# Kernel optimization log

Hardware: AMD Instinct MI355X
Metric: run time of the kernel (lower is better)

## Reference

```python
import jax, jax.numpy as jnp
import numpy as np
import math

H = 16
D_MODEL = 1024
D_K = 64
BS = 8
SEQ = 1024


def setup_inputs() -> dict:
    key = jax.random.key(0)
    ks = jax.random.split(key, 13)
    s = 1.0 / math.sqrt(D_MODEL)
    inp = {
        "q": jax.random.normal(ks[0], (BS, SEQ, D_MODEL), dtype=jnp.float32),
        "k": jax.random.normal(ks[1], (BS, SEQ, D_MODEL), dtype=jnp.float32),
        "v": jax.random.normal(ks[2], (BS, SEQ, D_MODEL), dtype=jnp.float32),
        "mask": jax.random.randint(ks[3], (BS, SEQ, SEQ), 0, 2, dtype=jnp.int32),
        "Wq": jax.random.normal(ks[4], (D_MODEL, D_MODEL), dtype=jnp.float32) * s,
        "bq": jax.random.normal(ks[5], (D_MODEL,), dtype=jnp.float32) * s,
        "Wk": jax.random.normal(ks[6], (D_MODEL, D_MODEL), dtype=jnp.float32) * s,
        "bk": jax.random.normal(ks[7], (D_MODEL,), dtype=jnp.float32) * s,
        "Wv": jax.random.normal(ks[8], (D_MODEL, D_MODEL), dtype=jnp.float32) * s,
        "bv": jax.random.normal(ks[9], (D_MODEL,), dtype=jnp.float32) * s,
        "Wo": jax.random.normal(ks[10], (D_MODEL, D_MODEL), dtype=jnp.float32) * s,
        "bo": jax.random.normal(ks[11], (D_MODEL,), dtype=jnp.float32) * s,
    }
    return inp


def reference(q, k, v, mask, Wq, bq, Wk, bk, Wv, bv, Wo, bo):
    bs, seq, _ = q.shape
    # projections, split heads: [b, h, s, dk]
    def proj(x, W, b):
        y = x @ W + b
        return y.reshape(bs, seq, H, D_K).transpose(0, 2, 1, 3)
    qh = proj(q, Wq, bq)
    kh = proj(k, Wk, bk)
    vh = proj(v, Wv, bv)
    # scaled dot-product attention (dropout is identity in eval mode)
    scores = jnp.einsum("bhqd,bhkd->bhqk", qh, kh) / math.sqrt(D_K)
    scores = jnp.where(mask[:, None, :, :] == 0, jnp.float32(-1e9), scores)
    attn = jax.nn.softmax(scores, axis=-1)
    ctx = jnp.einsum("bhqk,bhkd->bhqd", attn, vh)
    concat = ctx.transpose(0, 2, 1, 3).reshape(bs, seq, D_MODEL)
    return concat @ Wo + bo
```

## Files before the change

### kernel.cpp

```cpp
#include <hip/hip_runtime.h>
#include <hip/hip_bf16.h>

#define HN 16
#define DM 1024
#define DK 64
#define BSZ 8
#define SEQL 1024

typedef __attribute__((ext_vector_type(8))) short bf16x8;
typedef __attribute__((ext_vector_type(4))) short short4v;
typedef __attribute__((ext_vector_type(4))) float f32x4;

__device__ __forceinline__ short f2bf(float f) {
    union { float f; unsigned u; } x; x.f = f;
    unsigned u = x.u + 0x7FFFu + ((x.u >> 16) & 1u);
    return (short)(u >> 16);
}

__device__ __forceinline__ void async16(const void* g, void* ldsbase) {
    __builtin_amdgcn_global_load_lds(
        (const __attribute__((address_space(1))) unsigned int*)g,
        (__attribute__((address_space(3))) unsigned int*)ldsbase, 16, 0, 0);
}

__device__ __forceinline__ short4v pack4bf(float v0, float v1, float v2, float v3) {
    unsigned pk0, pk1;
    asm("v_cvt_pk_bf16_f32 %0, %1, %2" : "=v"(pk0) : "v"(v0), "v"(v1));
    asm("v_cvt_pk_bf16_f32 %0, %1, %2" : "=v"(pk1) : "v"(v2), "v"(v3));
    union { unsigned u[2]; short4v s4; } u_;
    u_.u[0] = pk0; u_.u[1] = pk1;
    return u_.s4;
}

__device__ __forceinline__ bf16x8 pack8bf(f32x4 lo, f32x4 hi) {
    union { short4v h[2]; bf16x8 v; } u_;
    u_.h[0] = pack4bf(lo.x, lo.y, lo.z, lo.w);
    u_.h[1] = pack4bf(hi.x, hi.y, hi.z, hi.w);
    return u_.v;
}

__global__ __launch_bounds__(256) void transpose_cast4(const float* __restrict__ W0,
                                                       const float* __restrict__ W1,
                                                       const float* __restrict__ W2,
                                                       const float* __restrict__ W3,
                                                       short* __restrict__ T0,
                                                       short* __restrict__ T1,
                                                       short* __restrict__ T2,
                                                       short* __restrict__ T3) {
    __shared__ float tile[32][33];
    const int zi = blockIdx.z;
    const float* W = zi == 0 ? W0 : zi == 1 ? W1 : zi == 2 ? W2 : W3;
    short* Wt = zi == 0 ? T0 : zi == 1 ? T1 : zi == 2 ? T2 : T3;
    const int t = threadIdx.x;
    const int k0 = blockIdx.x * 32, n0 = blockIdx.y * 32;
    const int c = t & 31, r = t >> 5;
    #pragma unroll
    for (int p = 0; p < 4; ++p)
        tile[r + 8 * p][c] = W[(size_t)(k0 + r + 8 * p) * DM + n0 + c];
    __syncthreads();
    #pragma unroll
    for (int p = 0; p < 4; ++p)
        Wt[(size_t)(n0 + r + 8 * p) * DM + k0 + c] = f2bf(tile[c][r + 8 * p]);
}

__global__ __launch_bounds__(256) void pack_mask(const int* __restrict__ mask,
                                                 unsigned short* __restrict__ bt) {
    size_t gi = (size_t)blockIdx.x * 256 + threadIdx.x;
    size_t word = gi >> 6;
    int l = threadIdx.x & 63;
    int jperm = ((l >> 2) & 3) * 16 + ((l >> 4) & 3) * 4 + (l & 3);
    size_t row = word >> 4;
    int jblk = (int)(word & 15);
    unsigned long long b = __ballot(mask[row * SEQL + jblk * 64 + jperm] != 0);
    if (l < 4)
        bt[row * 64 + l * 16 + jblk] = (unsigned short)(b >> (l * 16));
}

__global__ __launch_bounds__(256) void gemm_qkv(
    const float* __restrict__ Aq, const float* __restrict__ Ak,
    const float* __restrict__ Av,
    const short* __restrict__ Wqt, const short* __restrict__ Wkt,
    const short* __restrict__ Wvt,
    const float* __restrict__ bqp, const float* __restrict__ bkp,
    const float* __restrict__ bvp,
    short* __restrict__ Cq, short* __restrict__ Ck, short* __restrict__ Cv,
    int zlog) {
    __shared__ __attribute__((aligned(16))) float Af[2][128][32];
    __shared__ __attribute__((aligned(16))) short Bs[2][128][32];
    const int t = threadIdx.x;
    const int lane = t & 63, wv = t >> 6;
    const int wm = (wv >> 1) * 64, wn = (wv & 1) * 64;
    const int quad = lane >> 4, l15 = lane & 15;
    const int tileM = blockIdx.x * 128, tileN = blockIdx.y * 128;
    const int which = blockIdx.z >> zlog;
    const int zz = blockIdx.z & ((1 << zlog) - 1);
    const size_t zoff = (size_t)zz * DM * SEQL;
    const float* A = (which == 0 ? Aq : which == 1 ? Ak : Av) + zoff;
    const short* Wt = which == 0 ? Wqt : which == 1 ? Wkt : Wvt;
    const float* bias = which == 0 ? bqp : which == 1 ? bkp : bvp;
    short* C = (which == 0 ? Cq : which == 1 ? Ck : Cv) + zoff;

    const int arow = t >> 3;
    const int acol = ((t & 7) ^ (arow & 7)) * 4;
    const float* asrc = A + (size_t)(tileM + arow) * DM + acol;
    const int brow = t >> 2;
    const int bcol = (t & 3) * 8;
    const short* bsrc = Wt + (size_t)(tileN + brow) * DM + bcol;

    f32x4 acc[4][4];
    #pragma unroll
    for (int i = 0; i < 4; ++i)
        #pragma unroll
        for (int j = 0; j < 4; ++j) acc[i][j] = {0.f, 0.f, 0.f, 0.f};

    #pragma unroll
    for (int p = 0; p < 4; ++p)
        async16(asrc + (size_t)(p * 32) * DM, &Af[0][p * 32 + wv * 8][0]);
    #pragma unroll
    for (int p = 0; p < 2; ++p)
        async16(bsrc + (size_t)(p * 64) * DM, &Bs[0][p * 64 + wv * 16][0]);
    __syncthreads();

    #pragma unroll 2
    for (int idx = 0; idx < DM / 32; ++idx) {
        const int cur = idx & 1;
        const int k0 = idx * 32;
        if (k0 + 32 < DM) {
            #pragma unroll
            for (int p = 0; p < 4; ++p)
                async16(asrc + (size_t)(p * 32) * DM + (k0 + 32),
                        &Af[cur ^ 1][p * 32 + wv * 8][0]);
            #pragma unroll
            for (int p = 0; p < 2; ++p)
                async16(bsrc + (size_t)(p * 64) * DM + (k0 + 32),
                        &Bs[cur ^ 1][p * 64 + wv * 16][0]);
        }

        bf16x8 a[4], b[4];
        #pragma unroll
        for (int i = 0; i < 4; ++i) {
            const int r = wm + i * 16 + l15;
            const int s = r & 7;
            f32x4 lo = *(const f32x4*)&Af[cur][r][((2 * quad) ^ s) * 4];
            f32x4 hi = *(const f32x4*)&Af[cur][r][((2 * quad + 1) ^ s) * 4];
            a[i] = pack8bf(lo, hi);
        }
        #pragma unroll
        for (int j = 0; j < 4; ++j)
            b[j] = *(const bf16x8*)&Bs[cur][wn + j * 16 + l15][quad * 8];
        #pragma unroll
        for (int i = 0; i < 4; ++i)
            #pragma unroll
            for (int j = 0; j < 4; ++j)
                acc[i][j] = __builtin_amdgcn_mfma_f32_16x16x32_bf16(a[i], b[j], acc[i][j], 0, 0, 0);

        __syncthreads();
    }

    if (which == 2) {
        #pragma unroll
        for (int i = 0; i < 4; ++i)
            #pragma unroll
            for (int j = 0; j < 4; ++j) {
                int rowb = tileM + wm + i * 16 + quad * 4;
                int col = tileN + wn + j * 16 + l15;
                float bb = bias[col];
                short4v s4 = pack4bf(acc[i][j][0] + bb, acc[i][j][1] + bb,
                                     acc[i][j][2] + bb, acc[i][j][3] + bb);
                *(short4v*)(C + (size_t)col * SEQL + rowb) = s4;
            }
    } else {
        #pragma unroll
        for (int i = 0; i < 4; ++i)
            #pragma unroll
            for (int j = 0; j < 4; ++j)
                #pragma unroll
                for (int rr = 0; rr < 4; ++rr) {
                    int row = tileM + wm + i * 16 + quad * 4 + rr;
                    int col = tileN + wn + j * 16 + l15;
                    float v = acc[i][j][rr] + bias[col];
                    C[((size_t)(col >> 6) * SEQL + row) * DK + (col & 63)] = f2bf(v);
                }
    }
}

__global__ __launch_bounds__(256) void gemm_out(const short* __restrict__ A,
                                                const short* __restrict__ Wt,
                                                const float* __restrict__ bias,
                                                float* __restrict__ Cp) {
    __shared__ __attribute__((aligned(16))) short As[2][128][32];
    __shared__ __attribute__((aligned(16))) short Bs[2][128][32];
    const int t = threadIdx.x;
    const int lane = t & 63, wv = t >> 6;
    const int wm = (wv >> 1) * 64, wn = (wv & 1) * 64;
    const int quad = lane >> 4, l15 = lane & 15;
    const int tileM = blockIdx.x * 128, tileN = blockIdx.y * 128;
    const size_t zoff = (size_t)blockIdx.z * DM * SEQL;
    const short* Az = A + zoff;

    const int sr = wv * 16 + (lane >> 2);
    const int sc = (lane & 3) * 8;
    const short* asrc = Az + (size_t)(tileM + sr) * DM + sc;
    const short* bsrc = Wt + (size_t)(tileN + sr) * DM + sc;

    f32x4 acc[4][4];
    #pragma unroll
    for (int i = 0; i < 4; ++i)
        #pragma unroll
        for (int j = 0; j < 4; ++j) acc[i][j] = {0.f, 0.f, 0.f, 0.f};

    #pragma unroll
    for (int p = 0; p < 2; ++p) {
        async16(asrc + (size_t)p * 64 * DM, &As[0][p * 64 + wv * 16][0]);
        async16(bsrc + (size_t)p * 64 * DM, &Bs[0][p * 64 + wv * 16][0]);
    }
    __syncthreads();

    #pragma unroll 2
    for (int idx = 0; idx < DM / 32; ++idx) {
        const int cur = idx & 1;
        const int k0 = idx * 32;
        if (k0 + 32 < DM) {
            #pragma unroll
            for (int p = 0; p < 2; ++p) {
                async16(asrc + (size_t)p * 64 * DM + (k0 + 32),
                        &As[cur ^ 1][p * 64 + wv * 16][0]);
                async16(bsrc + (size_t)p * 64 * DM + (k0 + 32),
                        &Bs[cur ^ 1][p * 64 + wv * 16][0]);
            }
        }

        bf16x8 a[4], b[4];
        #pragma unroll
        for (int i = 0; i < 4; ++i) a[i] = *(const bf16x8*)&As[cur][wm + i * 16 + l15][quad * 8];
        #pragma unroll
        for (int j = 0; j < 4; ++j) b[j] = *(const bf16x8*)&Bs[cur][wn + j * 16 + l15][quad * 8];
        #pragma unroll
        for (int i = 0; i < 4; ++i)
            #pragma unroll
            for (int j = 0; j < 4; ++j)
                acc[i][j] = __builtin_amdgcn_mfma_f32_16x16x32_bf16(a[i], b[j], acc[i][j], 0, 0, 0);

        __syncthreads();
    }

    float* C = Cp + zoff;
    #pragma unroll
    for (int i = 0; i < 4; ++i)
        #pragma unroll
        for (int j = 0; j < 4; ++j)
            #pragma unroll
            for (int rr = 0; rr < 4; ++rr) {
                int row = tileM + wm + i * 16 + quad * 4 + rr;
                int col = tileN + wn + j * 16 + l15;
                C[(size_t)row * DM + col] = acc[i][j][rr] + bias[col];
            }
}

template <bool USE_BITS>
__global__ __launch_bounds__(256) void attn_mfma(const short* __restrict__ Qw,
                                                 const short* __restrict__ Kw,
                                                 const short* __restrict__ Vt,
                                                 const void* __restrict__ maskp,
                                                 short* __restrict__ ctx) {
    __shared__ __attribute__((aligned(16))) short Kbuf[2][64 * 64];
    __shared__ __attribute__((aligned(16))) short Vbuf[2][64 * 64];
    __shared__ __attribute__((aligned(16))) short Ps[4][16 * 64];
    const int t = threadIdx.x;
    const int lane = t & 63, w = t >> 6;
    const int quad = lane >> 4, l15 = lane & 15;
    const int nwg = gridDim.x;
    const int cpx = nwg >> 3;
    const int vb = (blockIdx.x & 7) * cpx + (blockIdx.x >> 3);
    const int q0 = (vb & 15) * 64;
    const int h = (vb >> 4) & 15;
    const int z = vb >> 8;
    const size_t zoff = (size_t)z * DM * SEQL;
    const short* Qb = Qw + zoff + (size_t)h * SEQL * DK;
    const short* Kb = Kw + zoff + (size_t)h * SEQL * DK;
    const short* Vb = Vt + zoff + (size_t)h * DK * SEQL;
    const int qrow = q0 + w * 16 + l15;
    const int x = (l15 & 7) << 3;

    bf16x8 qf0 = *(const bf16x8*)(Qb + (size_t)qrow * DK + quad * 8);
    bf16x8 qf1 = *(const bf16x8*)(Qb + (size_t)qrow * DK + 32 + quad * 8);

    unsigned long long mA = 0, mB = 0, mC = 0, mD = 0;
    if (USE_BITS) {
        const unsigned long long* bt64 = (const unsigned long long*)
            ((const unsigned short*)maskp + (size_t)z * SEQL * 64 +
             (size_t)qrow * 64 + quad * 16);
        mA = bt64[0]; mB = bt64[1]; mC = bt64[2]; mD = bt64[3];
    }

    const int r0 = t >> 3;
    const int kc = ((t & 7) ^ (r0 & 7)) * 8;
    const short* ks0 = Kb + (size_t)r0 * DK + kc;
    const short* ks1 = ks0 + 32 * DK;
    const short* vs0 = Vb + (size_t)r0 * SEQL + kc;
    const short* vs1 = vs0 + 32 * SEQL;

    async16(ks0, &Kbuf[0][w * 512]);
    async16(ks1, &Kbuf[0][2048 + w * 512]);
    async16(vs0, &Vbuf[0][w * 512]);
    async16(vs1, &Vbuf[0][2048 + w * 512]);
    ks0 += 64 * DK; ks1 += 64 * DK; vs0 += 64; vs1 += 64;
    __syncthreads();

    f32x4 o[4];
    #pragma unroll
    for (int td = 0; td < 4; ++td) o[td] = {0.f, 0.f, 0.f, 0.f};
    float Lacc = 0.f;

    #pragma unroll 2
    for (int iter = 0; iter < 16; ++iter) {
        const int cur = iter & 1;
        if (iter < 15) {
            async16(ks0, &Kbuf[cur ^ 1][w * 512]);
            async16(ks1, &Kbuf[cur ^ 1][2048 + w * 512]);
            async16(vs0, &Vbuf[cur ^ 1][w * 512]);
            async16(vs1, &Vbuf[cur ^ 1][2048 + w * 512]);
            ks0 += 64 * DK; ks1 += 64 * DK; vs0 += 64; vs1 += 64;
        }

        const short* Kl = &Kbuf[cur][0];
        const short* Vl = &Vbuf[cur][0];
        unsigned mw16 = 0;
        if (USE_BITS) {
            unsigned long long t01 = (iter & 4) ? mB : mA;
            unsigned long long t23 = (iter & 4) ? mD : mC;
            unsigned long long tw = (iter & 8) ? t23 : t01;
            mw16 = (unsigned)(tw >> ((iter & 3) * 16)) & 0xFFFFu;
        }

        #pragma unroll
        for (int tn = 0; tn < 4; ++tn) {
            const int r = tn * 16 + l15;
            bf16x8 ak0 = *(const bf16x8*)&Kl[r * 64 + ((quad * 8) ^ x)];
            bf16x8 ak1 = *(const bf16x8*)&Kl[r * 64 + ((32 + quad * 8) ^ x)];
            f32x4 s = {0.f, 0.f, 0.f, 0.f};
            __builtin_amdgcn_s_setprio(1);
            s = __builtin_amdgcn_mfma_f32_16x16x32_bf16(ak0, qf0, s, 0, 0, 0);
            s = __builtin_amdgcn_mfma_f32_16x16x32_bf16(ak1, qf1, s, 0, 0, 0);
            __builtin_amdgcn_s_setprio(0);
            float pv[4];
            const unsigned nib = USE_BITS ? (mw16 >> (tn * 4)) & 0xFu : 0u;
            #pragma unroll
            for (int rr = 0; rr < 4; ++rr) {
                bool keep;
                if (USE_BITS) {
                    keep = (nib >> rr) & 1u;
                } else {
                    const int* mi = (const int*)maskp + (size_t)z * SEQL * SEQL;
                    keep = mi[(size_t)qrow * SEQL + iter * 64 + tn * 16 + quad * 4 + rr] != 0;
                }
                float e = __expf(s[rr] * 0.125f);
                pv[rr] = keep ? e : 0.0f;
                Lacc += pv[rr];
            }
            *(short4v*)&Ps[w][l15 * 64 + ((tn * 16 + quad * 4) ^ x)] =
                pack4bf(pv[0], pv[1], pv[2], pv[3]);
        }
        bf16x8 ap0 = *(const bf16x8*)&Ps[w][l15 * 64 + ((quad * 8) ^ x)];
        bf16x8 ap1 = *(const bf16x8*)&Ps[w][l15 * 64 + ((32 + quad * 8) ^ x)];
        __builtin_amdgcn_s_setprio(1);
        #pragma unroll
        for (int td = 0; td < 4; ++td) {
            const int r = td * 16 + l15;
            bf16x8 bv0 = *(const bf16x8*)&Vl[r * 64 + ((quad * 8) ^ x)];
            bf16x8 bv1 = *(const bf16x8*)&Vl[r * 64 + ((32 + quad * 8) ^ x)];
            o[td] = __builtin_amdgcn_mfma_f32_16x16x32_bf16(ap0, bv0, o[td], 0, 0, 0);
            o[td] = __builtin_amdgcn_mfma_f32_16x16x32_bf16(ap1, bv1, o[td], 0, 0, 0);
        }
        __builtin_amdgcn_s_setprio(0);

        __syncthreads();
    }

    Lacc += __shfl_xor(Lacc, 16);
    Lacc += __shfl_xor(Lacc, 32);
    float Linv = 1.0f / Lacc;
    float Linv4[4];
    #pragma unroll
    for (int rr = 0; rr < 4; ++rr)
        Linv4[rr] = __shfl(Linv, quad * 4 + rr);

    short* cb = ctx + zoff;
    #pragma unroll
    for (int td = 0; td < 4; ++td)
        #pragma unroll
        for (int rr = 0; rr < 4; ++rr) {
            int rq = q0 + w * 16 + quad * 4 + rr;
            int cd = h * 64 + td * 16 + l15;
            cb[(size_t)rq * DM + cd] = f2bf(o[td][rr] * Linv4[rr]);
        }
}

extern "C" void kernel_launch(void* const* d_in, const int* in_sizes, int n_in,
                              void* d_out, int out_size, void* d_ws, size_t ws_size,
                              hipStream_t stream) {
    const float* q  = (const float*)d_in[0];
    const float* k  = (const float*)d_in[1];
    const float* v  = (const float*)d_in[2];
    const int* mask = (const int*)d_in[3];
    const float* Wq = (const float*)d_in[4];
    const float* bq = (const float*)d_in[5];
    const float* Wk = (const float*)d_in[6];
    const float* bk = (const float*)d_in[7];
    const float* Wv = (const float*)d_in[8];
    const float* bv = (const float*)d_in[9];
    const float* Wo = (const float*)d_in[10];
    const float* bo = (const float*)d_in[11];
    float* out = (float*)d_out;

    const size_t MB = (size_t)1 << 20;
    const size_t MEL = (size_t)1024 * 1024;
    char* base = (char*)d_ws;

    short* Wqt = (short*)(base + 0 * 2 * MB);
    short* Wkt = (short*)(base + 1 * 2 * MB);
    short* Wvt = (short*)(base + 2 * 2 * MB);
    short* Wot = (short*)(base + 3 * 2 * MB);

    int zdim;
    bool use_bits;
    if      (ws_size >= 74 * MB) { zdim = 8; use_bits = true; }
    else if (ws_size >= 42 * MB) { zdim = 4; use_bits = true; }
    else if (ws_size >= 26 * MB) { zdim = 2; use_bits = true; }
    else if (ws_size >= 18 * MB) { zdim = 1; use_bits = true; }
    else                         { zdim = 1; use_bits = false; }
    const int zlog = (zdim == 8) ? 3 : (zdim == 4) ? 2 : (zdim == 2) ? 1 : 0;

    unsigned short* bits = (unsigned short*)(base + 8 * MB);
    char* bufs = base + (use_bits ? 9 : 8) * MB;
    const size_t bufB = (size_t)zdim * 2 * MB;
    short* Qw  = (short*)(bufs);
    short* Kw  = (short*)(bufs + bufB);
    short* Vw  = (short*)(bufs + 2 * bufB);
    short* ctx = (short*)(bufs + 3 * bufB);

    transpose_cast4<<<dim3(32, 32, 4), 256, 0, stream>>>(Wq, Wk, Wv, Wo,
                                                         Wqt, Wkt, Wvt, Wot);
    if (use_bits)
        pack_mask<<<(BSZ * SEQL * SEQL) / 256, 256, 0, stream>>>(mask, bits);

    const int iters = BSZ / zdim;
    for (int it = 0; it < iters; ++it) {
        const size_t boff = (size_t)it * zdim * MEL;
        const float* qb = q + boff;
        const float* kb = k + boff;
        const float* vb = v + boff;
        float* ob = out + boff;
        const void* mb = use_bits
            ? (const void*)(bits + (size_t)it * zdim * SEQL * 64)
            : (const void*)(mask + (size_t)it * zdim * SEQL * SEQL);

        gemm_qkv<<<dim3(8, 8, 3 * zdim), 256, 0, stream>>>(
            qb, kb, vb, Wqt, Wkt, Wvt, bq, bk, bv, Qw, Kw, Vw, zlog);

        const int attnBlocks = 16 * 16 * zdim;
        if (use_bits)
            attn_mfma<true><<<attnBlocks, 256, 0, stream>>>(Qw, Kw, Vw, mb, ctx);
        else
            attn_mfma<false><<<attnBlocks, 256, 0, stream>>>(Qw, Kw, Vw, mb, ctx);

        gemm_out<<<dim3(8, 8, zdim), 256, 0, stream>>>(ctx, Wot, bo, ob);
    }
}
```

Measured before the change: 395.5 us.

## Split fused QKV GEMM, fold softmax scale into Q, widen out-GEMM K tile

The fused three-way QKV projection and four-way transpose launches are split into separate per-matrix launches. The Q projection is pre-scaled by log2(e)/sqrt(dk) so attention can use raw v_exp_f32 without a multiply. The output GEMM now moves 64-wide K slabs with XOR swizzling, halving loop iterations and barriers. setprio hints around the attention MFMAs are removed. More launches add overhead and lose cross-matrix parallelism, and the exp2 trick relies on the folded scale being exact enough in bf16.

```diff
diff --git a/kernel.cpp b/kernel.cpp
--- a/kernel.cpp
+++ b/kernel.cpp
@@ -6,6 +6,7 @@
 #define DK 64
 #define BSZ 8
 #define SEQL 1024
+#define QSCALE 0.18033688f
 
 typedef __attribute__((ext_vector_type(8))) short bf16x8;
 typedef __attribute__((ext_vector_type(4))) short short4v;
@@ -39,18 +40,9 @@
     return u_.v;
 }
 
-__global__ __launch_bounds__(256) void transpose_cast4(const float* __restrict__ W0,
-                                                       const float* __restrict__ W1,
-                                                       const float* __restrict__ W2,
-                                                       const float* __restrict__ W3,
-                                                       short* __restrict__ T0,
-                                                       short* __restrict__ T1,
-                                                       short* __restrict__ T2,
-                                                       short* __restrict__ T3) {
+__global__ __launch_bounds__(256) void transpose_cast(const float* __restrict__ W,
+                                                      short* __restrict__ Wt) {
     __shared__ float tile[32][33];
-    const int zi = blockIdx.z;
-    const float* W = zi == 0 ? W0 : zi == 1 ? W1 : zi == 2 ? W2 : W3;
-    short* Wt = zi == 0 ? T0 : zi == 1 ? T1 : zi == 2 ? T2 : T3;
     const int t = threadIdx.x;
     const int k0 = blockIdx.x * 32, n0 = blockIdx.y * 32;
     const int c = t & 31, r = t >> 5;
@@ -76,15 +68,12 @@
         bt[row * 64 + l * 16 + jblk] = (unsigned short)(b >> (l * 16));
 }
 
-__global__ __launch_bounds__(256) void gemm_qkv(
-    const float* __restrict__ Aq, const float* __restrict__ Ak,
-    const float* __restrict__ Av,
-    const short* __restrict__ Wqt, const short* __restrict__ Wkt,
-    const short* __restrict__ Wvt,
-    const float* __restrict__ bqp, const float* __restrict__ bkp,
-    const float* __restrict__ bvp,
-    short* __restrict__ Cq, short* __restrict__ Ck, short* __restrict__ Cv,
-    int zlog) {
+template <int MODE>
+__global__ __launch_bounds__(256) void gemm_f32a(const float* __restrict__ A,
+                                                 const short* __restrict__ Wt,
+                                                 const float* __restrict__ bias,
+                                                 short* __restrict__ Cp,
+                                                 float cscale) {
     __shared__ __attribute__((aligned(16))) float Af[2][128][32];
     __shared__ __attribute__((aligned(16))) short Bs[2][128][32];
     const int t = threadIdx.x;
@@ -92,17 +81,13 @@
     const int wm = (wv >> 1) * 64, wn = (wv & 1) * 64;
     const int quad = lane >> 4, l15 = lane & 15;
     const int tileM = blockIdx.x * 128, tileN = blockIdx.y * 128;
-    const int which = blockIdx.z >> zlog;
-    const int zz = blockIdx.z & ((1 << zlog) - 1);
-    const size_t zoff = (size_t)zz * DM * SEQL;
-    const float* A = (which == 0 ? Aq : which == 1 ? Ak : Av) + zoff;
-    const short* Wt = which == 0 ? Wqt : which == 1 ? Wkt : Wvt;
-    const float* bias = which == 0 ? bqp : which == 1 ? bkp : bvp;
-    short* C = (which == 0 ? Cq : which == 1 ? Ck : Cv) + zoff;
+    const size_t zoff = (size_t)blockIdx.z * DM * SEQL;
+    const float* Az = A + zoff;
+    short* C = Cp + zoff;
 
     const int arow = t >> 3;
     const int acol = ((t & 7) ^ (arow & 7)) * 4;
-    const float* asrc = A + (size_t)(tileM + arow) * DM + acol;
+    const float* asrc = Az + (size_t)(tileM + arow) * DM + acol;
     const int brow = t >> 2;
     const int bcol = (t & 3) * 8;
     const short* bsrc = Wt + (size_t)(tileN + brow) * DM + bcol;
@@ -157,7 +142,7 @@
         __syncthreads();
     }
 
-    if (which == 2) {
+    if (MODE == 2) {
         #pragma unroll
         for (int i = 0; i < 4; ++i)
             #pragma unroll
@@ -178,7 +163,7 @@
                 for (int rr = 0; rr < 4; ++rr) {
                     int row = tileM + wm + i * 16 + quad * 4 + rr;
                     int col = tileN + wn + j * 16 + l15;
-                    float v = acc[i][j][rr] + bias[col];
+                    float v = (acc[i][j][rr] + bias[col]) * cscale;
                     C[((size_t)(col >> 6) * SEQL + row) * DK + (col & 63)] = f2bf(v);
                 }
     }
@@ -188,8 +173,8 @@
                                                 const short* __restrict__ Wt,
                                                 const float* __restrict__ bias,
                                                 float* __restrict__ Cp) {
-    __shared__ __attribute__((aligned(16))) short As[2][128][32];
-    __shared__ __attribute__((aligned(16))) short Bs[2][128][32];
+    __shared__ __attribute__((aligned(16))) short As[2][128][64];
+    __shared__ __attribute__((aligned(16))) short Bs[2][128][64];
     const int t = threadIdx.x;
     const int lane = t & 63, wv = t >> 6;
     const int wm = (wv >> 1) * 64, wn = (wv & 1) * 64;
@@ -197,11 +182,12 @@
     const int tileM = blockIdx.x * 128, tileN = blockIdx.y * 128;
     const size_t zoff = (size_t)blockIdx.z * DM * SEQL;
     const short* Az = A + zoff;
-
-    const int sr = wv * 16 + (lane >> 2);
-    const int sc = (lane & 3) * 8;
-    const short* asrc = Az + (size_t)(tileM + sr) * DM + sc;
-    const short* bsrc = Wt + (size_t)(tileN + sr) * DM + sc;
+    const int x = (l15 & 7) << 3;
+
+    const int r0 = t >> 3;
+    const int kc = ((t & 7) ^ (r0 & 7)) * 8;
+    const short* asrc = Az + (size_t)(tileM + r0) * DM + kc;
+    const short* bsrc = Wt + (size_t)(tileN + r0) * DM + kc;
 
     f32x4 acc[4][4];
     #pragma unroll
@@ -210,36 +196,42 @@
         for (int j = 0; j < 4; ++j) acc[i][j] = {0.f, 0.f, 0.f, 0.f};
 
     #pragma unroll
-    for (int p = 0; p < 2; ++p) {
-        async16(asrc + (size_t)p * 64 * DM, &As[0][p * 64 + wv * 16][0]);
-        async16(bsrc + (size_t)p * 64 * DM, &Bs[0][p * 64 + wv * 16][0]);
+    for (int p = 0; p < 4; ++p) {
+        async16(asrc + (size_t)(p * 32) * DM, &As[0][p * 32 + wv * 8][0]);
+        async16(bsrc + (size_t)(p * 32) * DM, &Bs[0][p * 32 + wv * 8][0]);
     }
     __syncthreads();
 
     #pragma unroll 2
-    for (int idx = 0; idx < DM / 32; ++idx) {
+    for (int idx = 0; idx < DM / 64; ++idx) {
         const int cur = idx & 1;
-        const int k0 = idx * 32;
-        if (k0 + 32 < DM) {
-            #pragma unroll
-            for (int p = 0; p < 2; ++p) {
-                async16(asrc + (size_t)p * 64 * DM + (k0 + 32),
-                        &As[cur ^ 1][p * 64 + wv * 16][0]);
-                async16(bsrc + (size_t)p * 64 * DM + (k0 + 32),
-                        &Bs[cur ^ 1][p * 64 + wv * 16][0]);
+        const int k0 = idx * 64;
+        if (k0 + 64 < DM) {
+            #pragma unroll
+            for (int p = 0; p < 4; ++p) {
+                async16(asrc + (size_t)(p * 32) * DM + (k0 + 64),
+                        &As[cur ^ 1][p * 32 + wv * 8][0]);
+                async16(bsrc + (size_t)(p * 32) * DM + (k0 + 64),
+                        &Bs[cur ^ 1][p * 32 + wv * 8][0]);
             }
         }
 
-        bf16x8 a[4], b[4];
-        #pragma unroll
-        for (int i = 0; i < 4; ++i) a[i] = *(const bf16x8*)&As[cur][wm + i * 16 + l15][quad * 8];
-        #pragma unroll
-        for (int j = 0; j < 4; ++j) b[j] = *(const bf16x8*)&Bs[cur][wn + j * 16 + l15][quad * 8];
-        #pragma unroll
-        for (int i = 0; i < 4; ++i)
+        #pragma unroll
+        for (int ks = 0; ks < 2; ++ks) {
+            const int off = (ks * 32 + quad * 8) ^ x;
+            bf16x8 a[4], b[4];
+            #pragma unroll
+            for (int i = 0; i < 4; ++i)
+                a[i] = *(const bf16x8*)&As[cur][wm + i * 16 + l15][off];
             #pragma unroll
             for (int j = 0; j < 4; ++j)
-                acc[i][j] = __builtin_amdgcn_mfma_f32_16x16x32_bf16(a[i], b[j], acc[i][j], 0, 0, 0);
+                b[j] = *(const bf16x8*)&Bs[cur][wn + j * 16 + l15][off];
+            #pragma unroll
+            for (int i = 0; i < 4; ++i)
+                #pragma unroll
+                for (int j = 0; j < 4; ++j)
+                    acc[i][j] = __builtin_amdgcn_mfma_f32_16x16x32_bf16(a[i], b[j], acc[i][j], 0, 0, 0);
+        }
 
         __syncthreads();
     }
@@ -339,10 +331,8 @@
             bf16x8 ak0 = *(const bf16x8*)&Kl[r * 64 + ((quad * 8) ^ x)];
             bf16x8 ak1 = *(const bf16x8*)&Kl[r * 64 + ((32 + quad * 8) ^ x)];
             f32x4 s = {0.f, 0.f, 0.f, 0.f};
-            __builtin_amdgcn_s_setprio(1);
             s = __builtin_amdgcn_mfma_f32_16x16x32_bf16(ak0, qf0, s, 0, 0, 0);
             s = __builtin_amdgcn_mfma_f32_16x16x32_bf16(ak1, qf1, s, 0, 0, 0);
-            __builtin_amdgcn_s_setprio(0);
             float pv[4];
             const unsigned nib = USE_BITS ? (mw16 >> (tn * 4)) & 0xFu : 0u;
             #pragma unroll
@@ -354,7 +344,8 @@
                     const int* mi = (const int*)maskp + (size_t)z * SEQL * SEQL;
                     keep = mi[(size_t)qrow * SEQL + iter * 64 + tn * 16 + quad * 4 + rr] != 0;
                 }
-                float e = __expf(s[rr] * 0.125f);
+                float e;
+                asm("v_exp_f32 %0, %1" : "=v"(e) : "v"(s[rr]));
                 pv[rr] = keep ? e : 0.0f;
                 Lacc += pv[rr];
             }
@@ -363,7 +354,6 @@
         }
         bf16x8 ap0 = *(const bf16x8*)&Ps[w][l15 * 64 + ((quad * 8) ^ x)];
         bf16x8 ap1 = *(const bf16x8*)&Ps[w][l15 * 64 + ((32 + quad * 8) ^ x)];
-        __builtin_amdgcn_s_setprio(1);
         #pragma unroll
         for (int td = 0; td < 4; ++td) {
             const int r = td * 16 + l15;
@@ -372,7 +362,6 @@
             o[td] = __builtin_amdgcn_mfma_f32_16x16x32_bf16(ap0, bv0, o[td], 0, 0, 0);
             o[td] = __builtin_amdgcn_mfma_f32_16x16x32_bf16(ap1, bv1, o[td], 0, 0, 0);
         }
-        __builtin_amdgcn_s_setprio(0);
 
         __syncthreads();
     }
@@ -429,7 +418,6 @@
     else if (ws_size >= 26 * MB) { zdim = 2; use_bits = true; }
     else if (ws_size >= 18 * MB) { zdim = 1; use_bits = true; }
     else                         { zdim = 1; use_bits = false; }
-    const int zlog = (zdim == 8) ? 3 : (zdim == 4) ? 2 : (zdim == 2) ? 1 : 0;
 
     unsigned short* bits = (unsigned short*)(base + 8 * MB);
     char* bufs = base + (use_bits ? 9 : 8) * MB;
@@ -439,8 +427,10 @@
     short* Vw  = (short*)(bufs + 2 * bufB);
     short* ctx = (short*)(bufs + 3 * bufB);
 
-    transpose_cast4<<<dim3(32, 32, 4), 256, 0, stream>>>(Wq, Wk, Wv, Wo,
-                                                         Wqt, Wkt, Wvt, Wot);
+    transpose_cast<<<dim3(32, 32), 256, 0, stream>>>(Wq, Wqt);
+    transpose_cast<<<dim3(32, 32), 256, 0, stream>>>(Wk, Wkt);
+    transpose_cast<<<dim3(32, 32), 256, 0, stream>>>(Wv, Wvt);
+    transpose_cast<<<dim3(32, 32), 256, 0, stream>>>(Wo, Wot);
     if (use_bits)
         pack_mask<<<(BSZ * SEQL * SEQL) / 256, 256, 0, stream>>>(mask, bits);
 
@@ -455,8 +445,9 @@
             ? (const void*)(bits + (size_t)it * zdim * SEQL * 64)
             : (const void*)(mask + (size_t)it * zdim * SEQL * SEQL);
 
-        gemm_qkv<<<dim3(8, 8, 3 * zdim), 256, 0, stream>>>(
-            qb, kb, vb, Wqt, Wkt, Wvt, bq, bk, bv, Qw, Kw, Vw, zlog);
+        gemm_f32a<0><<<dim3(8, 8, zdim), 256, 0, stream>>>(qb, Wqt, bq, Qw, QSCALE);
+        gemm_f32a<0><<<dim3(8, 8, zdim), 256, 0, stream>>>(kb, Wkt, bk, Kw, 1.0f);
+        gemm_f32a<2><<<dim3(8, 8, zdim), 256, 0, stream>>>(vb, Wvt, bv, Vw, 1.0f);
 
         const int attnBlocks = 16 * 16 * zdim;
         if (use_bits)
```

Result: no change. 389.7 us (-1.5%).
